# Optimization experiments

Hardware: AMD Instinct MI355X
Metric: run time of the kernel (lower is better)

## Reference

```python
import jax, jax.numpy as jnp
import numpy as np

T, B, I, H = 256, 128, 512, 1024

def setup_inputs() -> dict:
    key = jax.random.key(0)
    k1, k2, k3, k4, k5 = jax.random.split(key, 5)
    s_ih = 1.0 / np.sqrt(H)
    return {
        "x": jax.random.normal(k1, (T, B, I), dtype=jnp.float32),
        "hidden": jnp.zeros((B, H), dtype=jnp.float32),
        "W_ih": jax.random.uniform(k2, (H, I), jnp.float32, -s_ih, s_ih),
        "W_hh": jax.random.uniform(k3, (H, H), jnp.float32, -s_ih, s_ih),
        "b_ih": jax.random.uniform(k4, (H,), jnp.float32, -s_ih, s_ih),
        "b_hh": jax.random.uniform(k5, (H,), jnp.float32, -s_ih, s_ih),
    }

def reference(x, hidden, W_ih, W_hh, b_ih, b_hh):
    # Faithful to the source: forward() applies the RNNCell to the SAME
    # initial hidden at every timestep (hidden is never updated in the loop).
    # out[t] = relu(x[t] @ W_ih^T + b_ih + hidden @ W_hh^T + b_hh)
    h_term = hidden @ W_hh.T + b_hh          # (B, H), shared across time
    pre = jnp.einsum('tbi,hi->tbh', x, W_ih) + b_ih + h_term  # (T, B, H)
    out = jax.nn.relu(pre)
    return out, out[-1]
```

## Files before the change

### kernel.cpp

```cpp
#include <hip/hip_runtime.h>
#include <hip/hip_bf16.h>

#define T_DIM 256
#define B_DIM 128
#define I_DIM 512
#define H_DIM 1024

typedef __attribute__((ext_vector_type(4))) float f32x4;
typedef __attribute__((ext_vector_type(8))) short short8;

__device__ inline unsigned short f2bf(float f) {
    __hip_bfloat16 h = __float2bfloat16(f);
    unsigned short u;
    __builtin_memcpy(&u, &h, sizeof(u));
    return u;
}

template <int MODE>
__global__ __launch_bounds__(256, 2) void gemm_bt(
    const float* __restrict__ A, const float* __restrict__ Bm,
    int M, int N, int K,
    const float* __restrict__ bias0, const float* __restrict__ bias1,
    float* __restrict__ C, float* __restrict__ Clast) {
    __shared__ unsigned short As[128 * 64];
    __shared__ unsigned short Bs[128 * 64];

    const int tid = threadIdx.x;
    const int wid = tid >> 6;
    const int lane = tid & 63;
    const int wr = wid >> 1, wc = wid & 1;
    const int lhi = lane >> 4;
    const int llo = lane & 15;

    const int orig = blockIdx.x;
    const int nwg = gridDim.x;
    const int wg = (nwg > 8 && (nwg & 7) == 0)
                       ? ((orig & 7) * (nwg >> 3) + (orig >> 3))
                       : orig;
    const int m0 = (wg >> 3) * 128;
    const int n0 = (wg & 7) * 128;

    const int srow = tid >> 3;
    const int c8 = tid & 7;
    const int slot8 = (c8 ^ (srow & 7)) * 8;

    const float* Aptr = A + (size_t)(m0 + srow) * K + c8 * 8;
    const float* Bptr = Bm + (size_t)(n0 + srow) * K + c8 * 8;

    f32x4 pf[2][4][2];

    auto issue = [&](int k0) {
#pragma unroll
        for (int g = 0; g < 4; ++g) {
            const float* pa = Aptr + (size_t)g * 32 * K + k0;
            const float* pb = Bptr + (size_t)g * 32 * K + k0;
            pf[0][g][0] = *(const f32x4*)pa;
            pf[0][g][1] = *(const f32x4*)(pa + 4);
            pf[1][g][0] = *(const f32x4*)pb;
            pf[1][g][1] = *(const f32x4*)(pb + 4);
        }
    };
    auto write_lds = [&]() {
#pragma unroll
        for (int g = 0; g < 4; ++g) {
            union { unsigned short s[8]; short8 v; } pka, pkb;
#pragma unroll
            for (int j = 0; j < 4; ++j) {
                pka.s[j] = f2bf(pf[0][g][0][j]);
                pka.s[4 + j] = f2bf(pf[0][g][1][j]);
                pkb.s[j] = f2bf(pf[1][g][0][j]);
                pkb.s[4 + j] = f2bf(pf[1][g][1][j]);
            }
            *(short8*)&As[(srow + g * 32) * 64 + slot8] = pka.v;
            *(short8*)&Bs[(srow + g * 32) * 64 + slot8] = pkb.v;
        }
    };

    f32x4 acc[4][4] = {};

    auto compute = [&]() {
#pragma unroll
        for (int ks = 0; ks < 2; ++ks) {
            short8 af[4], bfr[4];
#pragma unroll
            for (int mi = 0; mi < 4; ++mi) {
                int ar = wr * 64 + mi * 16 + llo;
                int slot = ((ks << 2) + lhi) ^ (ar & 7);
                af[mi] = *(const short8*)&As[ar * 64 + slot * 8];
            }
#pragma unroll
            for (int ni = 0; ni < 4; ++ni) {
                int br = wc * 64 + ni * 16 + llo;
                int slot = ((ks << 2) + lhi) ^ (br & 7);
                bfr[ni] = *(const short8*)&Bs[br * 64 + slot * 8];
            }
#pragma unroll
            for (int mi = 0; mi < 4; ++mi)
#pragma unroll
                for (int ni = 0; ni < 4; ++ni)
                    acc[mi][ni] = __builtin_amdgcn_mfma_f32_16x16x32_bf16(
                        af[mi], bfr[ni], acc[mi][ni], 0, 0, 0);
        }
    };

    issue(0);
    write_lds();
    __syncthreads();
    for (int k0 = 64; k0 < K; k0 += 64) {
        issue(k0);
        compute();
        __syncthreads();
        write_lds();
        __syncthreads();
    }
    compute();

    const bool last_tile = (m0 == M - 128);
#pragma unroll
    for (int mi = 0; mi < 4; ++mi) {
#pragma unroll
        for (int ni = 0; ni < 4; ++ni) {
            int col = n0 + wc * 64 + ni * 16 + llo;
            int rowb = m0 + wr * 64 + mi * 16 + lhi * 4;
            if (MODE == 0) {
                float bsum = bias0[col] + bias1[col];
#pragma unroll
                for (int r = 0; r < 4; ++r)
                    C[(size_t)(rowb + r) * N + col] = acc[mi][ni][r] + bsum;
            } else {
#pragma unroll
                for (int r = 0; r < 4; ++r) {
                    int row = rowb + r;
                    float v = acc[mi][ni][r] + bias0[(row & 127) * N + col];
                    v = fmaxf(v, 0.0f);
                    C[(size_t)row * N + col] = v;
                    if (last_tile) Clast[(row & 127) * N + col] = v;
                }
            }
        }
    }
}

extern "C" void kernel_launch(void* const* d_in, const int* in_sizes, int n_in,
                              void* d_out, int out_size, void* d_ws, size_t ws_size,
                              hipStream_t stream) {
    const float* x = (const float*)d_in[0];
    const float* hidden = (const float*)d_in[1];
    const float* W_ih = (const float*)d_in[2];
    const float* W_hh = (const float*)d_in[3];
    const float* b_ih = (const float*)d_in[4];
    const float* b_hh = (const float*)d_in[5];

    float* out = (float*)d_out;
    float* out_last = out + (size_t)T_DIM * B_DIM * H_DIM;
    float* biasall = (float*)d_ws;

    gemm_bt<0><<<dim3(H_DIM / 128), dim3(256), 0, stream>>>(
        hidden, W_hh, B_DIM, H_DIM, H_DIM, b_ih, b_hh, biasall, nullptr);
    gemm_bt<1><<<dim3((T_DIM * B_DIM) / 128 * (H_DIM / 128)), dim3(256), 0, stream>>>(
        x, W_ih, T_DIM * B_DIM, H_DIM, I_DIM, biasall, nullptr, out, out_last);
}
```

Baseline: 115.7 us.

## Pre-pack W_ih to bf16 tiles and stream operands via direct global-to-LDS loads

Adds a pre-pass that converts W_ih to bf16 in a pre-swizzled tile layout, and a new main GEMM that loads X (fp32) and the packed weights straight into LDS with global_load_lds. Conversion of X to bf16 now happens at fragment-read time from LDS. The goal is to remove register staging and repeated weight conversion across 256 M-tiles. In exchange the fp32 A tile doubles LDS use, and the loop has no double buffering, so each k-step waits for its loads. The old path is kept as a fallback when workspace is too small.

```diff
diff --git a/kernel.cpp b/kernel.cpp
--- a/kernel.cpp
+++ b/kernel.cpp
@@ -1,10 +1,12 @@
 #include <hip/hip_runtime.h>
 #include <hip/hip_bf16.h>
+#include <stdint.h>
 
 #define T_DIM 256
 #define B_DIM 128
 #define I_DIM 512
 #define H_DIM 1024
+#define M_DIM (T_DIM * B_DIM)
 
 typedef __attribute__((ext_vector_type(4))) float f32x4;
 typedef __attribute__((ext_vector_type(8))) short short8;
@@ -14,6 +16,121 @@
     unsigned short u;
     __builtin_memcpy(&u, &h, sizeof(u));
     return u;
+}
+
+__device__ inline void gload_lds16(const void* g, void* l) {
+    __builtin_amdgcn_global_load_lds(
+        (const __attribute__((address_space(1))) uint32_t*)g,
+        (__attribute__((address_space(3))) uint32_t*)l, 16, 0, 0);
+}
+
+__global__ void pack_W(const float* __restrict__ W, unsigned short* __restrict__ Wp) {
+    int id = blockIdx.x * 256 + threadIdx.x;
+    int s = id & 7;
+    int r = (id >> 3) & 127;
+    int kst = (id >> 10) & 7;
+    int nt = id >> 13;
+    int srcg = s ^ (r & 7);
+    const float* src = W + (size_t)(nt * 128 + r) * I_DIM + kst * 64 + srcg * 8;
+    f32x4 lo = *(const f32x4*)src;
+    f32x4 hi = *(const f32x4*)(src + 4);
+    union { unsigned short us[8]; short8 v; } pk;
+#pragma unroll
+    for (int j = 0; j < 4; ++j) { pk.us[j] = f2bf(lo[j]); pk.us[4 + j] = f2bf(hi[j]); }
+    *(short8*)(Wp + (size_t)id * 8) = pk.v;
+}
+
+__global__ __launch_bounds__(256, 3) void gemm_main(
+    const float* __restrict__ X, const unsigned short* __restrict__ Wp,
+    const float* __restrict__ biasall, float* __restrict__ C,
+    float* __restrict__ Clast) {
+    __shared__ float Asf[128 * 64];
+    __shared__ unsigned short Bsb[128 * 64];
+
+    const int tid = threadIdx.x;
+    const int lane = tid & 63;
+    const int wid = tid >> 6;
+    const int wr = wid >> 1, wc = wid & 1;
+    const int llo = lane & 15, lhi = lane >> 4;
+
+    const int orig = blockIdx.x;
+    const int nwg = gridDim.x;
+    const int wg = ((orig & 7) * (nwg >> 3)) + (orig >> 3);
+    const int mt = wg >> 3;
+    const int nt = wg & 7;
+    const int m0 = mt * 128;
+    const int n0 = nt * 128;
+
+    const int arow_l = tid >> 4;
+    const int csrc = (tid & 15) ^ arow_l;
+    const float* Abase = X + (size_t)(m0 + arow_l) * I_DIM + csrc * 4;
+    const unsigned short* Bbase = Wp + (size_t)nt * 8 * 8192 + (size_t)tid * 8;
+
+    f32x4 acc[4][4] = {};
+
+#pragma unroll
+    for (int kst = 0; kst < I_DIM / 64; ++kst) {
+        if (kst) __syncthreads();
+        const float* asrc = Abase + kst * 64;
+#pragma unroll
+        for (int g = 0; g < 8; ++g)
+            gload_lds16(asrc + (size_t)g * 16 * I_DIM,
+                        (char*)Asf + (g * 256 + tid) * 16);
+        const unsigned short* bsrc = Bbase + kst * 8192;
+#pragma unroll
+        for (int g = 0; g < 4; ++g)
+            gload_lds16(bsrc + g * 2048, (char*)Bsb + (g * 256 + tid) * 16);
+        __syncthreads();
+
+#pragma unroll
+        for (int ks = 0; ks < 2; ++ks) {
+            short8 af[4], bfv[4];
+#pragma unroll
+            for (int mi = 0; mi < 4; ++mi) {
+                int ar = wr * 64 + mi * 16 + llo;
+                int g0 = ks * 8 + lhi * 2;
+                f32x4 a0 = *(const f32x4*)&Asf[ar * 64 + ((g0 ^ (ar & 15)) << 2)];
+                f32x4 a1 = *(const f32x4*)&Asf[ar * 64 + (((g0 + 1) ^ (ar & 15)) << 2)];
+                union { unsigned short s[8]; short8 v; } pk;
+#pragma unroll
+                for (int j = 0; j < 4; ++j) {
+                    pk.s[j] = f2bf(a0[j]);
+                    pk.s[4 + j] = f2bf(a1[j]);
+                }
+                af[mi] = pk.v;
+            }
+#pragma unroll
+            for (int ni = 0; ni < 4; ++ni) {
+                int br = wc * 64 + ni * 16 + llo;
+                int g = ks * 4 + lhi;
+                bfv[ni] = *(const short8*)&Bsb[br * 64 + ((g ^ (br & 7)) << 3)];
+            }
+#pragma unroll
+            for (int mi = 0; mi < 4; ++mi)
+#pragma unroll
+                for (int ni = 0; ni < 4; ++ni)
+                    acc[mi][ni] = __builtin_amdgcn_mfma_f32_16x16x32_bf16(
+                        af[mi], bfv[ni], acc[mi][ni], 0, 0, 0);
+        }
+    }
+
+    const bool last_tile = (m0 == M_DIM - 128);
+#pragma unroll
+    for (int mi = 0; mi < 4; ++mi) {
+#pragma unroll
+        for (int ni = 0; ni < 4; ++ni) {
+            int col = n0 + wc * 64 + ni * 16 + llo;
+            int rowb = m0 + wr * 64 + mi * 16 + lhi * 4;
+#pragma unroll
+            for (int r = 0; r < 4; ++r) {
+                int row = rowb + r;
+                float v = acc[mi][ni][r] + biasall[(row & 127) * H_DIM + col];
+                v = fmaxf(v, 0.0f);
+                C[(size_t)row * H_DIM + col] = v;
+                if (last_tile) Clast[(row & 127) * H_DIM + col] = v;
+            }
+        }
+    }
 }
 
 template <int MODE>
@@ -153,10 +270,20 @@
 
     float* out = (float*)d_out;
     float* out_last = out + (size_t)T_DIM * B_DIM * H_DIM;
+
     float* biasall = (float*)d_ws;
+    unsigned short* Wp = (unsigned short*)((char*)d_ws + 512 * 1024);
+    const size_t ws_need = 512 * 1024 + (size_t)H_DIM * I_DIM * 2;
 
     gemm_bt<0><<<dim3(H_DIM / 128), dim3(256), 0, stream>>>(
         hidden, W_hh, B_DIM, H_DIM, H_DIM, b_ih, b_hh, biasall, nullptr);
-    gemm_bt<1><<<dim3((T_DIM * B_DIM) / 128 * (H_DIM / 128)), dim3(256), 0, stream>>>(
-        x, W_ih, T_DIM * B_DIM, H_DIM, I_DIM, biasall, nullptr, out, out_last);
-}
+
+    if (ws_size >= ws_need) {
+        pack_W<<<dim3(H_DIM * I_DIM / 8 / 256), dim3(256), 0, stream>>>(W_ih, Wp);
+        gemm_main<<<dim3(M_DIM / 128 * (H_DIM / 128)), dim3(256), 0, stream>>>(
+            x, Wp, biasall, out, out_last);
+    } else {
+        gemm_bt<1><<<dim3(M_DIM / 128 * (H_DIM / 128)), dim3(256), 0, stream>>>(
+            x, W_ih, M_DIM, H_DIM, I_DIM, biasall, nullptr, out, out_last);
+    }
+}
```

After: 109.9 us. -5.0%, faster.
